# Kernel optimization log

Hardware: AMD Instinct MI355X
Metric: run time of the kernel (lower is better)

## Reference

```python
import jax, jax.numpy as jnp
import numpy as np

T = 1_000_000      # number of feature rows
D = 82             # STSIM feature dim (hardcoded Linear(82, 1))
NUM_GROUPS = 256   # N = mask.max() + 1 in the original (fixed for jit)


def setup_inputs() -> dict:
    key = jax.random.key(0)
    k1, k2, k3, k4, k5 = jax.random.split(key, 5)
    X1 = jax.random.normal(k1, (T, D), jnp.float32)
    X2 = jax.random.normal(k2, (T, D), jnp.float32)
    Y = jax.random.normal(k3, (T,), jnp.float32)
    mask = jax.random.randint(k4, (T,), 0, NUM_GROUPS)
    # Linear(82,1,bias=False) weight; positive (matches init_weight = 1/var)
    # so sqrt(M((X1-X2)^2)) is real.
    W = jax.random.uniform(k5, (1, D), jnp.float32, 0.01, 1.0)
    return {"X1": X1, "X2": X2, "Y": Y, "W": W, "mask": mask}


def _criterion(x, Y, mask):
    # Vectorized version of the per-group Pearson-correlation loop:
    # one pass of segment reductions instead of N full-array boolean masks.
    seg = lambda v: jax.ops.segment_sum(v, mask, num_segments=NUM_GROUPS)
    counts = seg(jnp.ones_like(x))                      # [N]
    xc = x - (seg(x) / counts)[mask]                    # per-group centered
    yc = Y - (seg(Y) / counts)[mask]
    nom = seg(xc * yc)                                  # [N]
    denom = jnp.sqrt(seg(xc * xc) * seg(yc * yc))       # [N]
    return jnp.sum(jnp.abs(nom / denom)) / NUM_GROUPS


def reference(X1, X2, Y, W, mask):
    # pred = sqrt(Linear((X1 - X2)^2))  -> [T, 1]
    pred = jnp.sqrt(((X1 - X2) ** 2) @ W.T)
    coeff = _criterion(pred[:, 0], Y, mask)
    return coeff, pred
```

## Files before the change

kernel.cpp:

```cpp
#include <hip/hip_runtime.h>

#define T_ROWS   1000000
#define D        82
#define NG       256
#define RPC      64
#define CHB      20992
#define NCHUNKS  15625
#define NBLOCKS  256

#define WSD_CNT 0
#define WSD_SP  256
#define WSD_SPP 512
#define WSD_SY  768
#define WSD_SYY 1024
#define WSD_SPY 1280

typedef const __attribute__((address_space(1))) unsigned int* gp1_t;
typedef __attribute__((address_space(3))) unsigned int* lp3_t;

__device__ __forceinline__ void gl16(const void* g, const void* l) {
    __builtin_amdgcn_global_load_lds((gp1_t)(unsigned long long)g,
                                     (lp3_t)(unsigned int)(unsigned long long)l,
                                     16, 0, 0);
}

__global__ __launch_bounds__(256) void fused_kernel(
    const float* __restrict__ X1, const float* __restrict__ X2,
    const float* __restrict__ Y,  const float* __restrict__ W,
    const int* __restrict__ mask, float* __restrict__ pred_out,
    double* __restrict__ wsd)
{
    __shared__ __align__(16) float sbuf[3][10496];
    __shared__ float t_cnt[NG], t_sp[NG], t_spp[NG], t_sy[NG], t_syy[NG], t_spy[NG];

    const int tid  = threadIdx.x;
    const int wid  = tid >> 6;
    const int lane = tid & 63;
    const int b    = blockIdx.x;

    t_cnt[tid] = 0.f; t_sp[tid]  = 0.f; t_spp[tid] = 0.f;
    t_sy[tid]  = 0.f; t_syy[tid] = 0.f; t_spy[tid] = 0.f;

    const int rloc = tid >> 2;
    const int q    = tid & 3;
    const int e0   = q * 20;
    float wreg[20];
    #pragma unroll
    for (int k = 0; k < 20; ++k) wreg[k] = W[e0 + k];
    float w20 = 0.f, w21 = 0.f;
    if (q == 3) { w20 = W[80]; w21 = W[81]; }

    __syncthreads();

    const int nJ = (NCHUNKS - b + 255) >> 8;

    auto stage = [&](int c, int bi) {
        const char* g1 = (const char*)X1 + (size_t)c * CHB;
        const char* g2 = (const char*)X2 + (size_t)c * CHB;
        char* l = (char*)&sbuf[bi][0];
        for (int s = wid; s < 21; s += 4) {
            if (s < 20) {
                gl16(g1 + s * 1024 + lane * 16, l + s * 1024);
                gl16(g2 + s * 1024 + lane * 16, l + CHB + s * 1024);
            } else if (lane < 32) {
                gl16(g1 + 20480 + lane * 16, l + 20480);
                gl16(g2 + 20480 + lane * 16, l + CHB + 20480);
            }
        }
    };

    int   mnext = 0; float ynext = 0.f;
    if (q == 0) { const int r0 = b * RPC + rloc; mnext = mask[r0]; ynext = Y[r0]; }

    stage(b, 0);
    stage(b + 256, 1);

    for (int j = 0; j < nJ; ++j) {
        const int c  = b + (j << 8);
        const int bi = j % 3;

        if (j == nJ - 1) asm volatile("s_waitcnt vmcnt(0)" ::: "memory");
        else             asm volatile("s_waitcnt vmcnt(10)" ::: "memory");
        __builtin_amdgcn_s_barrier();
        asm volatile("" ::: "memory");

        if (j + 2 < nJ) stage(b + ((j + 2) << 8), (j + 2) % 3);

        const int   mcur = mnext; const float ycur = ynext;
        if (q == 0 && j + 1 < nJ) {
            const int rn = (c + 256) * RPC + rloc;
            mnext = mask[rn]; ynext = Y[rn];
        }

        const float* row1 = &sbuf[bi][rloc * 82];
        const float* row2 = row1 + 5248;
        float acc = 0.f;
        #pragma unroll
        for (int k = 0; k < 20; k += 2) {
            const float2 a  = *(const float2*)(row1 + e0 + k);
            const float2 bb = *(const float2*)(row2 + e0 + k);
            const float d0 = a.x - bb.x, d1 = a.y - bb.y;
            acc += d0 * d0 * wreg[k];
            acc += d1 * d1 * wreg[k + 1];
        }
        if (q == 3) {
            const float2 a  = *(const float2*)(row1 + 80);
            const float2 bb = *(const float2*)(row2 + 80);
            const float d0 = a.x - bb.x, d1 = a.y - bb.y;
            acc += d0 * d0 * w20 + d1 * d1 * w21;
        }
        acc += __shfl_xor(acc, 1);
        acc += __shfl_xor(acc, 2);

        if (q == 0) {
            const float p = sqrtf(acc);
            pred_out[c * RPC + rloc] = p;
            const int g = mcur;
            atomicAdd(&t_cnt[g], 1.f);
            atomicAdd(&t_sp [g], p);
            atomicAdd(&t_spp[g], p * p);
            atomicAdd(&t_sy [g], ycur);
            atomicAdd(&t_syy[g], ycur * ycur);
            atomicAdd(&t_spy[g], p * ycur);
        }
    }

    __syncthreads();
    atomicAdd(&wsd[WSD_CNT + tid], (double)t_cnt[tid]);
    atomicAdd(&wsd[WSD_SP  + tid], (double)t_sp [tid]);
    atomicAdd(&wsd[WSD_SPP + tid], (double)t_spp[tid]);
    atomicAdd(&wsd[WSD_SY  + tid], (double)t_sy [tid]);
    atomicAdd(&wsd[WSD_SYY + tid], (double)t_syy[tid]);
    atomicAdd(&wsd[WSD_SPY + tid], (double)t_spy[tid]);
}

__global__ void final_kernel(const double* __restrict__ wsd, float* __restrict__ out)
{
    __shared__ float red[NG];
    const int g = threadIdx.x;
    const double n   = wsd[WSD_CNT + g];
    const double sp  = wsd[WSD_SP  + g];
    const double spp = wsd[WSD_SPP + g];
    const double sy  = wsd[WSD_SY  + g];
    const double syy = wsd[WSD_SYY + g];
    const double spy = wsd[WSD_SPY + g];
    const double sxy = spy - sp * sy / n;
    const double sxx = spp - sp * sp / n;
    const double syc = syy - sy * sy / n;
    red[g] = (float)fabs(sxy / sqrt(sxx * syc));
    __syncthreads();
    for (int s = 128; s > 0; s >>= 1) {
        if (g < s) red[g] += red[g + s];
        __syncthreads();
    }
    if (g == 0) out[0] = red[0] / (float)NG;
}

extern "C" void kernel_launch(void* const* d_in, const int* in_sizes, int n_in,
                              void* d_out, int out_size, void* d_ws, size_t ws_size,
                              hipStream_t stream)
{
    const float* X1   = (const float*)d_in[0];
    const float* X2   = (const float*)d_in[1];
    const float* Y    = (const float*)d_in[2];
    const float* W    = (const float*)d_in[3];
    const int*   mask = (const int*)d_in[4];
    float* out = (float*)d_out;

    hipMemsetAsync(d_ws, 0, 6 * NG * sizeof(double), stream);
    fused_kernel<<<NBLOCKS, 256, 0, stream>>>(X1, X2, Y, W, mask, out + 1, (double*)d_ws);
    final_kernel<<<1, NG, 0, stream>>>((const double*)d_ws, out);
}
```

Before: 642.2 us.

## Halve chunk size, double block count, spread global atomics across eight sets

Chunks shrink from 64 to 32 rows, so the grid doubles to 512 blocks and each row is now split across 8 lanes instead of 4, with one extra shuffle step. The aim is higher occupancy and more memory-level parallelism for this bandwidth-bound streaming kernel. LDS per block drops, which allows more resident blocks per CU, and the per-wave vmcnt waits are retuned for the smaller stage. The final double-precision atomics are spread over 8 workspace copies that the final kernel sums, which reduces contention in exchange for a larger memset.

After: 635.8 us. No clear change (-1.0%).

```diff
diff --git a/kernel.cpp b/kernel.cpp
--- a/kernel.cpp
+++ b/kernel.cpp
@@ -3,17 +3,20 @@
 #define T_ROWS   1000000
 #define D        82
 #define NG       256
-#define RPC      64
-#define CHB      20992
-#define NCHUNKS  15625
-#define NBLOCKS  256
+#define RPC      32
+#define CHB      10496
+#define CHF      2624
+#define NCHUNKS  31250
+#define NBLOCKS  512
+#define NSET     8
 
+#define SET_STRIDE (6 * NG)
 #define WSD_CNT 0
-#define WSD_SP  256
-#define WSD_SPP 512
-#define WSD_SY  768
-#define WSD_SYY 1024
-#define WSD_SPY 1280
+#define WSD_SP  (1 * NG)
+#define WSD_SPP (2 * NG)
+#define WSD_SY  (3 * NG)
+#define WSD_SYY (4 * NG)
+#define WSD_SPY (5 * NG)
 
 typedef const __attribute__((address_space(1))) unsigned int* gp1_t;
 typedef __attribute__((address_space(3))) unsigned int* lp3_t;
@@ -30,7 +33,7 @@
     const int* __restrict__ mask, float* __restrict__ pred_out,
     double* __restrict__ wsd)
 {
-    __shared__ __align__(16) float sbuf[3][10496];
+    __shared__ __align__(16) float sbuf[3][2 * CHF];
     __shared__ float t_cnt[NG], t_sp[NG], t_spp[NG], t_sy[NG], t_syy[NG], t_spy[NG];
 
     const int tid  = threadIdx.x;
@@ -41,76 +44,79 @@
     t_cnt[tid] = 0.f; t_sp[tid]  = 0.f; t_spp[tid] = 0.f;
     t_sy[tid]  = 0.f; t_syy[tid] = 0.f; t_spy[tid] = 0.f;
 
-    const int rloc = tid >> 2;
-    const int q    = tid & 3;
-    const int e0   = q * 20;
-    float wreg[20];
+    const int rloc = tid >> 3;
+    const int q    = tid & 7;
+    const int e0   = q * 10;
+    float wreg[10];
     #pragma unroll
-    for (int k = 0; k < 20; ++k) wreg[k] = W[e0 + k];
-    float w20 = 0.f, w21 = 0.f;
-    if (q == 3) { w20 = W[80]; w21 = W[81]; }
+    for (int k = 0; k < 10; ++k) wreg[k] = W[e0 + k];
+    float w80 = 0.f, w81 = 0.f;
+    if (q == 7) { w80 = W[80]; w81 = W[81]; }
 
     __syncthreads();
 
-    const int nJ = (NCHUNKS - b + 255) >> 8;
+    const int nJ = (NCHUNKS - b + NBLOCKS - 1) / NBLOCKS;
 
     auto stage = [&](int c, int bi) {
         const char* g1 = (const char*)X1 + (size_t)c * CHB;
         const char* g2 = (const char*)X2 + (size_t)c * CHB;
         char* l = (char*)&sbuf[bi][0];
-        for (int s = wid; s < 21; s += 4) {
-            if (s < 20) {
+        #pragma unroll
+        for (int s0 = 0; s0 < 3; ++s0) {
+            const int s = wid + 4 * s0;
+            if (s < 10) {
                 gl16(g1 + s * 1024 + lane * 16, l + s * 1024);
                 gl16(g2 + s * 1024 + lane * 16, l + CHB + s * 1024);
-            } else if (lane < 32) {
-                gl16(g1 + 20480 + lane * 16, l + 20480);
-                gl16(g2 + 20480 + lane * 16, l + CHB + 20480);
+            } else if (s == 10 && lane < 16) {
+                gl16(g1 + 10240 + lane * 16, l + 10240);
+                gl16(g2 + 10240 + lane * 16, l + CHB + 10240);
             }
         }
     };
 
-    int   mnext = 0; float ynext = 0.f;
+    stage(b, 0);
+    int mnext = 0; float ynext = 0.f;
     if (q == 0) { const int r0 = b * RPC + rloc; mnext = mask[r0]; ynext = Y[r0]; }
-
-    stage(b, 0);
-    stage(b + 256, 1);
+    stage(b + NBLOCKS, 1);
 
     for (int j = 0; j < nJ; ++j) {
-        const int c  = b + (j << 8);
+        const int c  = b + j * NBLOCKS;
         const int bi = j % 3;
 
-        if (j == nJ - 1) asm volatile("s_waitcnt vmcnt(0)" ::: "memory");
-        else             asm volatile("s_waitcnt vmcnt(10)" ::: "memory");
+        if (j == nJ - 1)   asm volatile("s_waitcnt vmcnt(0)" ::: "memory");
+        else if (wid == 3) asm volatile("s_waitcnt vmcnt(4)" ::: "memory");
+        else               asm volatile("s_waitcnt vmcnt(6)" ::: "memory");
         __builtin_amdgcn_s_barrier();
         asm volatile("" ::: "memory");
 
-        if (j + 2 < nJ) stage(b + ((j + 2) << 8), (j + 2) % 3);
+        if (j + 2 < nJ) stage(b + (j + 2) * NBLOCKS, (j + 2) % 3);
 
         const int   mcur = mnext; const float ycur = ynext;
         if (q == 0 && j + 1 < nJ) {
-            const int rn = (c + 256) * RPC + rloc;
+            const int rn = (c + NBLOCKS) * RPC + rloc;
             mnext = mask[rn]; ynext = Y[rn];
         }
 
         const float* row1 = &sbuf[bi][rloc * 82];
-        const float* row2 = row1 + 5248;
+        const float* row2 = row1 + CHF;
         float acc = 0.f;
         #pragma unroll
-        for (int k = 0; k < 20; k += 2) {
+        for (int k = 0; k < 10; k += 2) {
             const float2 a  = *(const float2*)(row1 + e0 + k);
             const float2 bb = *(const float2*)(row2 + e0 + k);
             const float d0 = a.x - bb.x, d1 = a.y - bb.y;
             acc += d0 * d0 * wreg[k];
             acc += d1 * d1 * wreg[k + 1];
         }
-        if (q == 3) {
+        if (q == 7) {
             const float2 a  = *(const float2*)(row1 + 80);
             const float2 bb = *(const float2*)(row2 + 80);
             const float d0 = a.x - bb.x, d1 = a.y - bb.y;
-            acc += d0 * d0 * w20 + d1 * d1 * w21;
+            acc += d0 * d0 * w80 + d1 * d1 * w81;
         }
         acc += __shfl_xor(acc, 1);
         acc += __shfl_xor(acc, 2);
+        acc += __shfl_xor(acc, 4);
 
         if (q == 0) {
             const float p = sqrtf(acc);
@@ -126,24 +132,30 @@
     }
 
     __syncthreads();
-    atomicAdd(&wsd[WSD_CNT + tid], (double)t_cnt[tid]);
-    atomicAdd(&wsd[WSD_SP  + tid], (double)t_sp [tid]);
-    atomicAdd(&wsd[WSD_SPP + tid], (double)t_spp[tid]);
-    atomicAdd(&wsd[WSD_SY  + tid], (double)t_sy [tid]);
-    atomicAdd(&wsd[WSD_SYY + tid], (double)t_syy[tid]);
-    atomicAdd(&wsd[WSD_SPY + tid], (double)t_spy[tid]);
+    double* dst = wsd + (size_t)(b & (NSET - 1)) * SET_STRIDE;
+    atomicAdd(&dst[WSD_CNT + tid], (double)t_cnt[tid]);
+    atomicAdd(&dst[WSD_SP  + tid], (double)t_sp [tid]);
+    atomicAdd(&dst[WSD_SPP + tid], (double)t_spp[tid]);
+    atomicAdd(&dst[WSD_SY  + tid], (double)t_sy [tid]);
+    atomicAdd(&dst[WSD_SYY + tid], (double)t_syy[tid]);
+    atomicAdd(&dst[WSD_SPY + tid], (double)t_spy[tid]);
 }
 
 __global__ void final_kernel(const double* __restrict__ wsd, float* __restrict__ out)
 {
     __shared__ float red[NG];
     const int g = threadIdx.x;
-    const double n   = wsd[WSD_CNT + g];
-    const double sp  = wsd[WSD_SP  + g];
-    const double spp = wsd[WSD_SPP + g];
-    const double sy  = wsd[WSD_SY  + g];
-    const double syy = wsd[WSD_SYY + g];
-    const double spy = wsd[WSD_SPY + g];
+    double n = 0, sp = 0, spp = 0, sy = 0, syy = 0, spy = 0;
+    #pragma unroll
+    for (int s = 0; s < NSET; ++s) {
+        const double* t = wsd + (size_t)s * SET_STRIDE;
+        n   += t[WSD_CNT + g];
+        sp  += t[WSD_SP  + g];
+        spp += t[WSD_SPP + g];
+        sy  += t[WSD_SY  + g];
+        syy += t[WSD_SYY + g];
+        spy += t[WSD_SPY + g];
+    }
     const double sxy = spy - sp * sy / n;
     const double sxx = spp - sp * sp / n;
     const double syc = syy - sy * sy / n;
@@ -167,7 +179,7 @@
     const int*   mask = (const int*)d_in[4];
     float* out = (float*)d_out;
 
-    hipMemsetAsync(d_ws, 0, 6 * NG * sizeof(double), stream);
+    hipMemsetAsync(d_ws, 0, NSET * SET_STRIDE * sizeof(double), stream);
     fused_kernel<<<NBLOCKS, 256, 0, stream>>>(X1, X2, Y, W, mask, out + 1, (double*)d_ws);
     final_kernel<<<1, NG, 0, stream>>>((const double*)d_ws, out);
 }
```
